# Optimization experiments

Measured on AMD Instinct MI355X. Metric: run time of the kernel, lower is better.

## Reference

```python
import jax, jax.numpy as jnp
import numpy as np

E = 256  # embedding_dim
H = 256  # hidden_dim
B = 65536


def setup_inputs() -> dict:
    key = jax.random.key(0)
    ks = jax.random.split(key, 15)
    inp = {
        "x": jax.random.normal(ks[0], (B, E), dtype=jnp.float32),
        "c": jax.random.normal(ks[1], (B, H), dtype=jnp.float32),
        "h": jax.random.normal(ks[2], (B, H), dtype=jnp.float32),
    }
    names = ["W_i", "U_i", "b_i", "W_f", "U_f", "b_f", "W_c", "U_c", "b_c", "W_o", "U_o", "b_o"]
    shapes = [(E, H), (H, H), (H,)] * 4
    for n, s, k in zip(names, shapes, ks[3:]):
        inp[n] = jax.random.normal(k, s, dtype=jnp.float32)
    return inp


def reference(x, c, h, W_i, U_i, b_i, W_f, U_f, b_f, W_c, U_c, b_c, W_o, U_o, b_o):
    # Batch the four input/hidden projections into two GEMMs, then fuse gates.
    W = jnp.concatenate([W_f, W_i, W_o, W_c], axis=1)  # [E, 4H]
    U = jnp.concatenate([U_f, U_i, U_o, U_c], axis=1)  # [H, 4H]
    b = jnp.concatenate([b_f, b_i, b_o, b_c], axis=0)  # [4H]
    z = x @ W + h @ U + b                               # [B, 4H]
    zf, zi, zo, zg = jnp.split(z, 4, axis=1)
    f = jax.nn.sigmoid(zf)
    i = jax.nn.sigmoid(zi)
    o = jax.nn.sigmoid(zo)
    g = jnp.tanh(zg)
    c_new = c * f + g * i
    h_new = o * jnp.tanh(c_new)
    return (c_new, h_new)
```

## Files before the change

### kernel.cpp

```cpp
#include <hip/hip_runtime.h>
#include <hip/hip_fp16.h>

typedef _Float16 half8 __attribute__((ext_vector_type(8)));
typedef float f32x4 __attribute__((ext_vector_type(4)));

#define BHSZ 16777216
#define SBAR() __builtin_amdgcn_s_barrier()

__device__ __forceinline__ void gload16(const void* g, const void* lds) {
  __builtin_amdgcn_global_load_lds((const __attribute__((address_space(1))) void*)g,
                                   (__attribute__((address_space(3))) void*)lds,
                                   16, 0, 0);
}

__device__ __forceinline__ float fast_sigmoid(float z) {
  float e = __builtin_amdgcn_exp2f(-z * 1.4426950408889634f);
  return __builtin_amdgcn_rcpf(1.0f + e);
}

__device__ __forceinline__ float fast_tanh(float z) {
  float a = __builtin_fabsf(z);
  float e = __builtin_amdgcn_exp2f(a * 2.8853900817779268f);
  float t = 1.0f - 2.0f * __builtin_amdgcn_rcpf(1.0f + e);
  return z < 0.0f ? -t : t;
}

__global__ __launch_bounds__(256) void pack_a(const float* __restrict__ x,
                                              const float* __restrict__ h,
                                              _Float16* __restrict__ Apk) {
  long i = (long)blockIdx.x * 256 + threadIdx.x;
  long e = i * 8;
  int b = (int)(e >> 9);
  int k = (int)(e & 511);
  const float* src = (k < 256) ? (x + (long)b * 256 + k)
                               : (h + (long)b * 256 + (k - 256));
  float4 v0 = reinterpret_cast<const float4*>(src)[0];
  float4 v1 = reinterpret_cast<const float4*>(src)[1];
  half8 o;
  o[0] = (_Float16)v0.x; o[1] = (_Float16)v0.y;
  o[2] = (_Float16)v0.z; o[3] = (_Float16)v0.w;
  o[4] = (_Float16)v1.x; o[5] = (_Float16)v1.y;
  o[6] = (_Float16)v1.z; o[7] = (_Float16)v1.w;
  *reinterpret_cast<half8*>(Apk + e) = o;
}

__global__ __launch_bounds__(256) void pack_b(
    const float* __restrict__ Wf, const float* __restrict__ Uf,
    const float* __restrict__ Wi, const float* __restrict__ Ui,
    const float* __restrict__ Wo, const float* __restrict__ Uo,
    const float* __restrict__ Wc, const float* __restrict__ Uc,
    _Float16* __restrict__ Bp) {
  int idx = blockIdx.x * 256 + threadIdx.x;
  int k = idx & 511;
  int Np = idx >> 9;
  int g = (Np >> 4) & 3;
  int cl = ((Np >> 6) << 4) | (Np & 15);
  const float* W;
  const float* U;
  switch (g) {
    case 0: W = Wf; U = Uf; break;
    case 1: W = Wi; U = Ui; break;
    case 2: W = Wo; U = Uo; break;
    default: W = Wc; U = Uc; break;
  }
  float v = (k < 256) ? W[k * 256 + cl] : U[(k - 256) * 256 + cl];
  Bp[idx] = (_Float16)v;
}

__global__ __launch_bounds__(512, 4) void lstm_gemm(
    const _Float16* __restrict__ Apk, const _Float16* __restrict__ Bp,
    const float* __restrict__ cin,
    const float* __restrict__ bf_, const float* __restrict__ bi_,
    const float* __restrict__ bo_, const float* __restrict__ bc_,
    float* __restrict__ out) {
  __shared__ __align__(16) char smem[73728];

  int tid = threadIdx.x;
  int w = tid >> 6, l = tid & 63;
  int l15 = l & 15, lg = l >> 4;
  int wr = w >> 1, wcn = w & 1;

  int bid = blockIdx.x;
  int wg = (bid & 7) * 256 + (bid >> 3);
  int bm = wg >> 3, bn = wg & 7;

  int rpl = tid >> 3, s8 = tid & 7;
  int i8 = s8 ^ (rpl & 7);
  int rbase = 2 * rpl + (i8 >> 2);
  int csrc = (i8 & 3) * 8;
  long sA = ((long)bm * 256 + rbase) * 512 + csrc;
  long sB = ((long)bn * 128 + rbase) * 512 + csrc;
  int wb1k = w * 1024;

  int offA[4], offB[4];
#pragma unroll
  for (int mf = 0; mf < 4; ++mf) {
    int r = wr * 64 + mf * 16 + l15;
    int rp = r >> 1;
    offA[mf] = rp * 128 + (((((r & 1) << 2) | lg) ^ (rp & 7)) << 4);
  }
#pragma unroll
  for (int nf = 0; nf < 4; ++nf) {
    int r = wcn * 64 + nf * 16 + l15;
    int rp = r >> 1;
    offB[nf] = 16384 + rp * 128 + (((((r & 1) << 2) | lg) ^ (rp & 7)) << 4);
  }

  f32x4 acc[4][4];
#pragma unroll
  for (int a2 = 0; a2 < 4; ++a2)
#pragma unroll
    for (int b2 = 0; b2 < 4; ++b2)
      acc[a2][b2] = (f32x4){0.f, 0.f, 0.f, 0.f};

  auto stage = [&](int js) {
    char* db = smem + (js % 3) * 24576;
    long ko = (long)js * 32;
#pragma unroll
    for (int p = 0; p < 2; ++p)
      gload16(Apk + sA + ko + (long)p * 128 * 512, db + p * 8192 + wb1k);
    gload16(Bp + sB + ko, db + 16384 + wb1k);
  };

  stage(0);
  stage(1);

#pragma unroll
  for (int j = 0; j < 16; ++j) {
    if (j <= 14)
      asm volatile("s_waitcnt vmcnt(3)" ::: "memory");
    else
      asm volatile("s_waitcnt vmcnt(0)" ::: "memory");
    SBAR();
    if (j <= 13) stage(j + 2);

    const char* sb = smem + (j % 3) * 24576;
    half8 bv[4], av[4];
#pragma unroll
    for (int nf = 0; nf < 4; ++nf)
      bv[nf] = *reinterpret_cast<const half8*>(sb + offB[nf]);
#pragma unroll
    for (int mf = 0; mf < 4; ++mf)
      av[mf] = *reinterpret_cast<const half8*>(sb + offA[mf]);
    __builtin_amdgcn_s_setprio(1);
#pragma unroll
    for (int mf = 0; mf < 4; ++mf)
#pragma unroll
      for (int nf = 0; nf < 4; ++nf)
        acc[mf][nf] = __builtin_amdgcn_mfma_f32_16x16x32_f16(
            av[mf], bv[nf], acc[mf][nf], 0, 0, 0);
    __builtin_amdgcn_s_setprio(0);
  }

  int col = (bn * 2 + wcn) * 16 + l15;
  float vbf = bf_[col], vbi = bi_[col], vbo = bo_[col], vbc = bc_[col];
#pragma unroll
  for (int mf = 0; mf < 4; ++mf) {
#pragma unroll
    for (int r = 0; r < 4; ++r) {
      long row = (long)(bm * 256 + wr * 64 + mf * 16 + lg * 4 + r);
      float zf = acc[mf][0][r] + vbf;
      float zi = acc[mf][1][r] + vbi;
      float zo = acc[mf][2][r] + vbo;
      float zg = acc[mf][3][r] + vbc;
      float fg = fast_sigmoid(zf);
      float ig = fast_sigmoid(zi);
      float og = fast_sigmoid(zo);
      float gg = fast_tanh(zg);
      float cv = cin[row * 256 + col];
      float cn = cv * fg + gg * ig;
      float hn = og * fast_tanh(cn);
      out[row * 256 + col] = cn;
      out[BHSZ + row * 256 + col] = hn;
    }
  }
}

extern "C" void kernel_launch(void* const* d_in, const int* in_sizes, int n_in,
                              void* d_out, int out_size, void* d_ws, size_t ws_size,
                              hipStream_t stream) {
  const float* x  = (const float*)d_in[0];
  const float* c  = (const float*)d_in[1];
  const float* h  = (const float*)d_in[2];
  const float* Wi = (const float*)d_in[3];
  const float* Ui = (const float*)d_in[4];
  const float* bi = (const float*)d_in[5];
  const float* Wf = (const float*)d_in[6];
  const float* Uf = (const float*)d_in[7];
  const float* bf = (const float*)d_in[8];
  const float* Wc = (const float*)d_in[9];
  const float* Uc = (const float*)d_in[10];
  const float* bc = (const float*)d_in[11];
  const float* Wo = (const float*)d_in[12];
  const float* Uo = (const float*)d_in[13];
  const float* bo = (const float*)d_in[14];

  _Float16* Apk = (_Float16*)d_ws;
  _Float16* Bp  = (_Float16*)((char*)d_ws + (size_t)65536 * 512 * 2);

  pack_a<<<16384, 256, 0, stream>>>(x, h, Apk);
  pack_b<<<2048, 256, 0, stream>>>(Wf, Uf, Wi, Ui, Wo, Uo, Wc, Uc, Bp);
  lstm_gemm<<<2048, 512, 0, stream>>>(Apk, Bp, c, bf, bi, bo, bc,
                                      (float*)d_out);
}
```

Baseline: 146.2 us.

## Load GEMM B operand directly into registers instead of staging through LDS

The weight (B) tile is no longer copied into shared memory with global_load_lds. Each wave now loads its own B fragments straight from global memory into a double-buffered register array, one k-step ahead. Only the A tile stays in the triple-buffered LDS pipeline, which cuts shared memory per block from 72KB to 48KB and removes the B LDS reads. The cost is redundant global/L2 reads of B across waves in the same column, more VGPRs, and wait counts that now depend on how loads are ordered, which scheduling barriers try to preserve.

```diff
diff --git a/kernel.cpp b/kernel.cpp
--- a/kernel.cpp
+++ b/kernel.cpp
@@ -6,6 +6,7 @@
 
 #define BHSZ 16777216
 #define SBAR() __builtin_amdgcn_s_barrier()
+#define SCHEDB() __builtin_amdgcn_sched_barrier(0)
 
 __device__ __forceinline__ void gload16(const void* g, const void* lds) {
   __builtin_amdgcn_global_load_lds((const __attribute__((address_space(1))) void*)g,
@@ -73,7 +74,7 @@
     const float* __restrict__ bf_, const float* __restrict__ bi_,
     const float* __restrict__ bo_, const float* __restrict__ bc_,
     float* __restrict__ out) {
-  __shared__ __align__(16) char smem[73728];
+  __shared__ __align__(16) char smem[49152];
 
   int tid = threadIdx.x;
   int w = tid >> 6, l = tid & 63;
@@ -89,21 +90,21 @@
   int rbase = 2 * rpl + (i8 >> 2);
   int csrc = (i8 & 3) * 8;
   long sA = ((long)bm * 256 + rbase) * 512 + csrc;
-  long sB = ((long)bn * 128 + rbase) * 512 + csrc;
   int wb1k = w * 1024;
 
-  int offA[4], offB[4];
+  int offA[4];
 #pragma unroll
   for (int mf = 0; mf < 4; ++mf) {
     int r = wr * 64 + mf * 16 + l15;
     int rp = r >> 1;
     offA[mf] = rp * 128 + (((((r & 1) << 2) | lg) ^ (rp & 7)) << 4);
   }
+
+  const _Float16* bBase[4];
 #pragma unroll
   for (int nf = 0; nf < 4; ++nf) {
-    int r = wcn * 64 + nf * 16 + l15;
-    int rp = r >> 1;
-    offB[nf] = 16384 + rp * 128 + (((((r & 1) << 2) | lg) ^ (rp & 7)) << 4);
+    int r = bn * 128 + wcn * 64 + nf * 16 + l15;
+    bBase[nf] = Bp + (long)r * 512 + lg * 8;
   }
 
   f32x4 acc[4][4];
@@ -113,42 +114,51 @@
     for (int b2 = 0; b2 < 4; ++b2)
       acc[a2][b2] = (f32x4){0.f, 0.f, 0.f, 0.f};
 
-  auto stage = [&](int js) {
-    char* db = smem + (js % 3) * 24576;
+  half8 breg[2][4];
+
+  auto stageA = [&](int js) {
+    char* db = smem + (js % 3) * 16384;
     long ko = (long)js * 32;
 #pragma unroll
     for (int p = 0; p < 2; ++p)
       gload16(Apk + sA + ko + (long)p * 128 * 512, db + p * 8192 + wb1k);
-    gload16(Bp + sB + ko, db + 16384 + wb1k);
   };
-
-  stage(0);
-  stage(1);
+  auto issueB = [&](int js, int s) {
+#pragma unroll
+    for (int nf = 0; nf < 4; ++nf)
+      breg[s][nf] = *reinterpret_cast<const half8*>(bBase[nf] + js * 32);
+  };
+
+  stageA(0);
+  SCHEDB();
+  issueB(0, 0);
+  SCHEDB();
+  stageA(1);
 
 #pragma unroll
   for (int j = 0; j < 16; ++j) {
     if (j <= 14)
-      asm volatile("s_waitcnt vmcnt(3)" ::: "memory");
+      asm volatile("s_waitcnt vmcnt(2)" ::: "memory");
     else
       asm volatile("s_waitcnt vmcnt(0)" ::: "memory");
     SBAR();
-    if (j <= 13) stage(j + 2);
-
-    const char* sb = smem + (j % 3) * 24576;
-    half8 bv[4], av[4];
-#pragma unroll
-    for (int nf = 0; nf < 4; ++nf)
-      bv[nf] = *reinterpret_cast<const half8*>(sb + offB[nf]);
+    if (j <= 14) issueB(j + 1, (j + 1) & 1);
+    SCHEDB();
+    if (j <= 13) stageA(j + 2);
+    SCHEDB();
+
+    const char* sa = smem + (j % 3) * 16384;
+    half8 av[4];
 #pragma unroll
     for (int mf = 0; mf < 4; ++mf)
-      av[mf] = *reinterpret_cast<const half8*>(sb + offA[mf]);
+      av[mf] = *reinterpret_cast<const half8*>(sa + offA[mf]);
     __builtin_amdgcn_s_setprio(1);
 #pragma unroll
     for (int mf = 0; mf < 4; ++mf)
 #pragma unroll
       for (int nf = 0; nf < 4; ++nf)
         acc[mf][nf] = __builtin_amdgcn_mfma_f32_16x16x32_f16(
-            av[mf], bv[nf], acc[mf][nf], 0, 0, 0);
+            av[mf], breg[j & 1][nf], acc[mf][nf], 0, 0, 0);
     __builtin_amdgcn_s_setprio(0);
   }
 
```

Measured after the change: 222.4 us. +52.1%, slower.
